# Kernel tuning notes

Measured on AMD Instinct MI355X. Metric: run time of the kernel, lower is better.

Reference implementation:

```python
import jax, jax.numpy as jnp
import numpy as np

EPS = 1e-5
B, C, T = 128, 64, 1000          # batch, EEG channels, time samples
NCLU, HID, NOUT = 8, 512, 4      # clusters, head hidden dim, outputs (=feature_dim)


def _conv1d(x, w):
    # x: (N, Cin, T), w: (Cout, Cin, K), valid conv along time
    return jax.lax.conv_general_dilated(x, w, (1,), 'VALID',
                                        dimension_numbers=('NCH', 'OIH', 'NCH'))


def _bn(x, g, b, m, v):
    # eval-mode BatchNorm over channel dim of (N, C, T)
    return (x - m[None, :, None]) * (g / jnp.sqrt(v + EPS))[None, :, None] + b[None, :, None]


def _pool3(x):
    # maxpool kernel 3 stride 3 along time
    return jax.lax.reduce_window(x, -jnp.inf, jax.lax.max, (1, 1, 3), (1, 1, 3), 'VALID')


def setup_inputs() -> dict:
    key = jax.random.key(0)
    ks = jax.random.split(key, 12)
    def nrm(k, shape, fan):
        return jax.random.normal(k, shape, jnp.float32) / np.float32(np.sqrt(fan))
    inp = {
        'x': jax.random.normal(ks[0], (B, C, T), jnp.float32),
        'cluster_ids': jax.random.randint(ks[1], (B,), 0, NCLU, jnp.int32),
        # Deep4Net-style backbone params
        'w_time': nrm(ks[2], (25, 1, 10), 10),
        'b_time': jnp.zeros((25,), jnp.float32),
        'w_spat': nrm(ks[3], (25, 25, C), 25 * C),
        'w2': nrm(ks[4], (50, 25, 10), 250),
        'w3': nrm(ks[5], (100, 50, 10), 500),
        'w4': nrm(ks[6], (200, 100, 10), 1000),
        'w_cls': nrm(ks[7], (NOUT, 200, 7), 1400),
        'b_cls': jnp.zeros((NOUT,), jnp.float32),
        # per-cluster expert head params
        'hW1': nrm(ks[8], (NCLU, HID, NOUT), NOUT),
        'hb1': jnp.zeros((NCLU, HID), jnp.float32),
        'hW2': nrm(ks[9], (NCLU, NOUT, HID), HID),
        'hb2': jnp.zeros((NCLU, NOUT), jnp.float32),
        'hg': jnp.ones((NCLU, HID), jnp.float32),
        'hbe': jnp.zeros((NCLU, HID), jnp.float32),
        'hm': jnp.zeros((NCLU, HID), jnp.float32),
        'hv': jnp.ones((NCLU, HID), jnp.float32),
    }
    for i, c in zip((1, 2, 3, 4), (25, 50, 100, 200)):
        inp[f'g{i}'] = jnp.ones((c,), jnp.float32)
        inp[f'be{i}'] = jnp.zeros((c,), jnp.float32)
        inp[f'm{i}'] = jnp.zeros((c,), jnp.float32)
        inp[f'v{i}'] = jnp.ones((c,), jnp.float32)
    return inp


def reference(x, cluster_ids, w_time, b_time, w_spat, w2, w3, w4, w_cls, b_cls,
              hW1, hb1, hW2, hb2, hg, hbe, hm, hv,
              g1, be1, m1, v1, g2, be2, m2, v2, g3, be3, m3, v3, g4, be4, m4, v4):
    b_, c_, t_ = x.shape
    # conv_time: same 25 temporal filters applied per EEG channel -> (B, C, 25, T1)
    h = _conv1d(x.reshape(b_ * c_, 1, t_), w_time) + b_time[None, :, None]
    h = h.reshape(b_, c_, 25, -1)
    # conv_spat: collapse EEG channel axis -> (B, 25, T1)
    z = jnp.einsum('bcft,gfc->bgt', h, w_spat)
    z = _pool3(jax.nn.elu(_bn(z, g1, be1, m1, v1)))
    for w, g, be, m, v in ((w2, g2, be2, m2, v2), (w3, g3, be3, m3, v3), (w4, g4, be4, m4, v4)):
        z = _pool3(jax.nn.elu(_bn(_conv1d(z, w), g, be, m, v)))
    # final_conv_length='auto': classifier conv reduces time dim to 1 -> (B, NOUT)
    feats = (_conv1d(z, w_cls) + b_cls[None, :, None])[:, :, 0]
    # per-sample expert head routing (Linear -> BN(eval) -> ReLU -> [Dropout eval] -> Linear)
    h1 = jnp.einsum('bf,bhf->bh', feats, hW1[cluster_ids]) + hb1[cluster_ids]
    h1 = (h1 - hm[cluster_ids]) * (hg[cluster_ids] / jnp.sqrt(hv[cluster_ids] + EPS)) + hbe[cluster_ids]
    h1 = jax.nn.relu(h1)
    return jnp.einsum('bh,boh->bo', h1, hW2[cluster_ids]) + hb2[cluster_ids]
```

## Files before the change

### kernel.cpp

```cpp
#include <hip/hip_runtime.h>
#include <math.h>

#define EPS_BN 1e-5f

typedef __attribute__((ext_vector_type(8))) short short8;
typedef __attribute__((ext_vector_type(4))) float f32x4;
typedef __attribute__((ext_vector_type(4))) unsigned int uint4v;

__device__ __forceinline__ unsigned short f2bf(float f) {
    unsigned int u = __float_as_uint(f);
    u = (u + 0x7fffu + ((u >> 16) & 1u)) >> 16;
    return (unsigned short)u;
}
__device__ __forceinline__ float bf2f(unsigned short s) {
    return __uint_as_float(((unsigned int)s) << 16);
}
__device__ __forceinline__ float elu1(float y) { return y > 0.f ? y : expm1f(y); }
__device__ __forceinline__ float warp_sum(float v) {
    for (int off = 32; off > 0; off >>= 1) v += __shfl_down(v, off);
    return v;
}

#define UW1 0
#define UW2 20480
#define UW3 40960
#define UW4 122880
#define BB1 0
#define BB2 32
#define BB3 96
#define BB4 224
#define Z1G_U 9192320
#define Z2G_U 10544000
#define Z3G_U 11420544

#define RS_ZB 36

__global__ __launch_bounds__(256) void kprep(
    const float* __restrict__ w_time, const float* __restrict__ b_time,
    const float* __restrict__ w_spat,
    const float* __restrict__ w2, const float* __restrict__ w3,
    const float* __restrict__ w4,
    const float* __restrict__ g1, const float* __restrict__ be1,
    const float* __restrict__ m1, const float* __restrict__ v1,
    const float* __restrict__ g2, const float* __restrict__ be2,
    const float* __restrict__ m2, const float* __restrict__ v2,
    const float* __restrict__ g3, const float* __restrict__ be3,
    const float* __restrict__ m3, const float* __restrict__ v3,
    const float* __restrict__ g4, const float* __restrict__ be4,
    const float* __restrict__ m4, const float* __restrict__ v4,
    unsigned short* __restrict__ wsz, float* __restrict__ biasf) {
    int idx = blockIdx.x * 256 + threadIdx.x;
    if (idx < 20480) {
        int k = idx >> 11, g = (idx >> 6) & 31, c = idx & 63;
        float val = 0.f;
        if (g < 25) {
            float s = 0.f;
#pragma unroll
            for (int f = 0; f < 25; ++f)
                s = fmaf(w_spat[g * 1600 + f * 64 + c], w_time[f * 10 + k], s);
            val = s * (g1[g] * rsqrtf(v1[g] + EPS_BN));
        }
        wsz[UW1 + idx] = f2bf(val);
    } else if (idx < 40960) {
        int j = idx - 20480;
        int k = j >> 11, g = (j >> 5) & 63, c = j & 31;
        float val = 0.f;
        if (g < 50 && c < 25)
            val = w2[(g * 25 + c) * 10 + k] * (g2[g] * rsqrtf(v2[g] + EPS_BN));
        wsz[UW2 + j] = f2bf(val);
    } else if (idx < 122880) {
        int j = idx - 40960;
        int k = j >> 13, g = (j >> 6) & 127, c = j & 63;
        float val = 0.f;
        if (g < 100 && c < 50)
            val = w3[(g * 50 + c) * 10 + k] * (g3[g] * rsqrtf(v3[g] + EPS_BN));
        wsz[UW3 + j] = f2bf(val);
    } else if (idx < 409600) {
        int j = idx - 122880;
        int k = j / 28672, r = j % 28672, g = r >> 7, c = r & 127;
        float val = 0.f;
        if (g < 200 && c < 100)
            val = w4[(g * 100 + c) * 10 + k] * (g4[g] * rsqrtf(v4[g] + EPS_BN));
        wsz[UW4 + j] = f2bf(val);
    } else if (idx < 410048) {
        int j = idx - 409600;
        if (j < 32) {
            int g = j; float val = 0.f;
            if (g < 25) {
                float beff = 0.f;
                for (int f = 0; f < 25; ++f) {
                    float a = 0.f;
                    for (int c = 0; c < 64; ++c) a += w_spat[g * 1600 + f * 64 + c];
                    beff = fmaf(a, b_time[f], beff);
                }
                float sc = g1[g] * rsqrtf(v1[g] + EPS_BN);
                val = be1[g] - m1[g] * sc + beff * sc;
            }
            biasf[BB1 + g] = val;
        } else if (j < 96) {
            int g = j - 32; float val = 0.f;
            if (g < 50) { float sc = g2[g] * rsqrtf(v2[g] + EPS_BN); val = be2[g] - m2[g] * sc; }
            biasf[BB2 + g] = val;
        } else if (j < 224) {
            int g = j - 96; float val = 0.f;
            if (g < 100) { float sc = g3[g] * rsqrtf(v3[g] + EPS_BN); val = be3[g] - m3[g] * sc; }
            biasf[BB3 + g] = val;
        } else {
            int g = j - 224; float val = 0.f;
            if (g < 200) { float sc = g4[g] * rsqrtf(v4[g] + EPS_BN); val = be4[g] - m4[g] * sc; }
            biasf[BB4 + g] = val;
        }
    }
}

template<int CPAD, int RS, int SP, int TT, int TPC, int NCHUNK, int JMAX,
         int GPAD, int TPOOL, int GSTORE, int NGV, int OUT_RS, bool OUT_F32,
         int KPRE>
__device__ __forceinline__ void conv_job(
    const unsigned short* xT, const unsigned short* __restrict__ wpk,
    const float* __restrict__ bias,
    unsigned short* zout, float* zoutf, unsigned short* zbw,
    int lane, int gbi, int po0) {
    const int lm = lane & 15, h8 = lane >> 4;
    const int gloc = lane & 31, hh = lane >> 5;

    f32x4 acc[TT][2];
#pragma unroll
    for (int i = 0; i < TT; ++i) {
        acc[i][0] = (f32x4){0.f, 0.f, 0.f, 0.f};
        acc[i][1] = (f32x4){0.f, 0.f, 0.f, 0.f};
    }

    const int abase = lm * RS + h8 * 8;
    const unsigned short* wp = wpk + (gbi * 32 + lm) * CPAD + h8 * 8;
#pragma unroll
    for (int ph = 0; ph < 10 / KPRE; ++ph) {
        short8 w0r[KPRE][SP], w1r[KPRE][SP];
#pragma unroll
        for (int kk = 0; kk < KPRE; ++kk) {
            const int k = ph * KPRE + kk;
#pragma unroll
            for (int s = 0; s < SP; ++s) {
                w0r[kk][s] = *(const short8*)(wp + k * (GPAD * CPAD) + s * 32);
                w1r[kk][s] = *(const short8*)(wp + k * (GPAD * CPAD) + 16 * CPAD + s * 32);
            }
        }
#pragma unroll
        for (int kk = 0; kk < KPRE; ++kk) {
            const int k = ph * KPRE + kk;
#pragma unroll
            for (int s = 0; s < SP; ++s) {
#pragma unroll
                for (int tt = 0; tt < TT; ++tt) {
                    short8 a = *(const short8*)&xT[abase + (tt * 16 + k) * RS + s * 32];
                    acc[tt][0] = __builtin_amdgcn_mfma_f32_16x16x32_bf16(
                        a, w0r[kk][s], acc[tt][0], 0, 0, 0);
                    acc[tt][1] = __builtin_amdgcn_mfma_f32_16x16x32_bf16(
                        a, w1r[kk][s], acc[tt][1], 0, 0, 0);
                }
            }
        }
    }

    const float bv0 = bias[gbi * 32 + lm];
    const float bv1 = bias[gbi * 32 + 16 + lm];
#pragma unroll
    for (int ch = 0; ch < NCHUNK; ++ch) {
#pragma unroll
        for (int ti = 0; ti < TPC; ++ti) {
            int ttg = ch * TPC + ti;
#pragma unroll
            for (int r = 0; r < 4; ++r) {
                float v0 = elu1(acc[ttg][0][r] + bv0);
                float v1 = elu1(acc[ttg][1][r] + bv1);
                int row = ti * 16 + 4 * h8 + r;
                zbw[row * RS_ZB + lm] = f2bf(v0);
                zbw[row * RS_ZB + 16 + lm] = f2bf(v1);
            }
        }
#pragma unroll
        for (int j = 0; j < JMAX; ++j) {
            int po = hh + 2 * j;
            if (3 * po + 2 < TPC * 16) {
                float q0 = bf2f(zbw[(3 * po) * RS_ZB + gloc]);
                float q1 = bf2f(zbw[(3 * po + 1) * RS_ZB + gloc]);
                float q2 = bf2f(zbw[(3 * po + 2) * RS_ZB + gloc]);
                float mx = fmaxf(q0, fmaxf(q1, q2));
                int poa = po0 + ch * 16 + po;
                int ga = gbi * 32 + gloc;
                if (poa < TPOOL && ga < GSTORE) {
                    if constexpr (OUT_F32)
                        zoutf[poa * OUT_RS + ga] = mx;
                    else
                        zout[poa * OUT_RS + ga] =
                            (ga < NGV) ? f2bf(mx) : (unsigned short)0;
                }
            }
        }
    }
}

__global__ __launch_bounds__(64) void ks1(
    const float* __restrict__ x,
    const unsigned short* __restrict__ wsu, const float* __restrict__ biasf,
    unsigned short* __restrict__ wsz) {
    __shared__ __align__(16) unsigned short xT[64 * 72];
    __shared__ __align__(16) unsigned short zb[48 * RS_ZB];
    const int b = blockIdx.x, tci = blockIdx.y, lane = threadIdx.x;
    const int t0 = tci * 48;
    const int cp = lane & 31, hf = lane >> 5;
    const float* xr0 = x + b * 64000 + (2 * cp) * 1000;
    const float* xr1 = xr0 + 1000;
#pragma unroll
    for (int q8 = 0; q8 < 8; ++q8) {
        const int q = hf * 8 + q8;
        const int tg = t0 + 4 * q;
        float4 va = {0.f, 0.f, 0.f, 0.f}, vb = {0.f, 0.f, 0.f, 0.f};
        if (tg + 4 <= 1000) {
            va = *(const float4*)(xr0 + tg);
            vb = *(const float4*)(xr1 + tg);
        } else if (tg < 1000) {
            float* pa = (float*)&va; float* pb = (float*)&vb;
#pragma unroll
            for (int e = 0; e < 4; ++e)
                if (tg + e < 1000) { pa[e] = xr0[tg + e]; pb[e] = xr1[tg + e]; }
        }
        const float* pa = (const float*)&va;
        const float* pb = (const float*)&vb;
#pragma unroll
        for (int e = 0; e < 4; ++e) {
            unsigned int pk = (unsigned int)f2bf(pa[e]) |
                              ((unsigned int)f2bf(pb[e]) << 16);
            *(unsigned int*)&xT[(4 * q + e) * 72 + 2 * cp] = pk;
        }
    }
    __syncthreads();
    conv_job<64, 72, 2, 3, 3, 1, 8, 32, 330, 32, 25, 32, false, 5>(
        xT, wsu + UW1, biasf + BB1,
        wsz + Z1G_U + b * 330 * 32, nullptr, zb, lane, 0, tci * 16);
}

__global__ __launch_bounds__(64) void ks2(
    const unsigned short* __restrict__ wsu, const float* __restrict__ biasf,
    unsigned short* __restrict__ wsz) {
    __shared__ __align__(16) unsigned short xT[64 * 40];
    __shared__ __align__(16) unsigned short zb[48 * RS_ZB];
    const int b = blockIdx.x, y = blockIdx.y, lane = threadIdx.x;
    const int gbi = y / 7, tci = y % 7, t0b = tci * 48;
    const unsigned short* z1g = wsz + Z1G_U + b * 330 * 32;
    for (int idx = lane; idx < 256; idx += 64) {
        int r = idx >> 2, q = idx & 3;
        uint4v v = {0u, 0u, 0u, 0u};
        if (t0b + r < 330) v = *(const uint4v*)&z1g[(t0b + r) * 32 + 8 * q];
        *(uint4v*)&xT[r * 40 + 8 * q] = v;
    }
    __syncthreads();
    conv_job<32, 40, 1, 3, 3, 1, 8, 64, 107, 64, 50, 64, false, 5>(
        xT, wsu + UW2, biasf + BB2,
        wsz + Z2G_U + b * 107 * 64, nullptr, zb, lane, gbi, tci * 16);
}

__global__ __launch_bounds__(64) void ks3(
    const unsigned short* __restrict__ wsu, const float* __restrict__ biasf,
    unsigned short* __restrict__ wsz) {
    __shared__ __align__(16) unsigned short z2t[64 * 72];
    __shared__ __align__(16) unsigned short zb[48 * RS_ZB];
    const int b = blockIdx.x, y = blockIdx.y, lane = threadIdx.x;
    const int gbi = y / 2, tci = y % 2, t0b = tci * 48;
    const unsigned short* z2g = wsz + Z2G_U + b * 107 * 64;
    for (int idx = lane; idx < 512; idx += 64) {
        int r = idx >> 3, q = idx & 7;
        uint4v v = {0u, 0u, 0u, 0u};
        if (t0b + r < 107) v = *(const uint4v*)&z2g[(t0b + r) * 64 + 8 * q];
        *(uint4v*)&z2t[r * 72 + 8 * q] = v;
    }
    __syncthreads();
    conv_job<64, 72, 2, 3, 3, 1, 8, 128, 32, 128, 100, 136, false, 5>(
        z2t, wsu + UW3, biasf + BB3,
        wsz + Z3G_U + b * 44 * 136, nullptr, zb, lane, gbi, tci * 16);
}

__global__ __launch_bounds__(448) void ks4h(
    const unsigned short* __restrict__ wsu, const float* __restrict__ biasf,
    const unsigned short* __restrict__ wsz,
    const float* __restrict__ w_cls, const float* __restrict__ b_cls,
    const int* __restrict__ cid,
    const float* __restrict__ hW1, const float* __restrict__ hb1,
    const float* __restrict__ hW2, const float* __restrict__ hb2,
    const float* __restrict__ hg, const float* __restrict__ hbe,
    const float* __restrict__ hm, const float* __restrict__ hv,
    float* __restrict__ out) {
    __shared__ __align__(16) unsigned short z3t[44 * 136];
    __shared__ __align__(16) unsigned short zb[7 * 32 * RS_ZB];
    __shared__ float z4f[1400];
    __shared__ float feats[4];
    __shared__ float h1s[512];
    const int b = blockIdx.x, t = threadIdx.x;
    const int lane = t & 63, wv = t >> 6;
    const unsigned short* z3g = wsz + Z3G_U + b * 44 * 136;
    for (int idx = t; idx < 748; idx += 448) {
        int r = idx / 17, q = idx % 17;
        uint4v v = {0u, 0u, 0u, 0u};
        if (r < 32) v = *(const uint4v*)&z3g[r * 136 + 8 * q];
        *(uint4v*)&z3t[r * 136 + 8 * q] = v;
    }
    __syncthreads();

    conv_job<128, 136, 4, 2, 2, 1, 4, 224, 7, 200, 200, 200, true, 5>(
        z3t, wsu + UW4, biasf + BB4,
        nullptr, z4f, zb + wv * (32 * RS_ZB), lane, wv, 0);
    __syncthreads();

    if (wv < 4) {
        float p = 0.f;
        for (int i = lane; i < 1400; i += 64) {
            int po = i / 200, g = i - po * 200;
            p = fmaf(z4f[i], w_cls[wv * 1400 + g * 7 + po], p);
        }
        p = warp_sum(p);
        if (lane == 0) feats[wv] = p + b_cls[wv];
    }
    __syncthreads();

    const int c = cid[b];
    const float f0 = feats[0], f1 = feats[1], f2 = feats[2], f3 = feats[3];
    for (int h = t; h < 512; h += 448) {
        const float* w1 = &hW1[(c * 512 + h) * 4];
        float v = f0 * w1[0] + f1 * w1[1] + f2 * w1[2] + f3 * w1[3] + hb1[c * 512 + h];
        float sc = hg[c * 512 + h] * rsqrtf(hv[c * 512 + h] + EPS_BN);
        v = (v - hm[c * 512 + h]) * sc + hbe[c * 512 + h];
        h1s[h] = fmaxf(v, 0.f);
    }
    __syncthreads();
    if (wv < 4) {
        float p = 0.f;
        for (int i = lane; i < 512; i += 64)
            p = fmaf(h1s[i], hW2[(c * 4 + wv) * 512 + i], p);
        p = warp_sum(p);
        if (lane == 0) out[b * 4 + wv] = p + hb2[c * 4 + wv];
    }
}

extern "C" void kernel_launch(void* const* d_in, const int* in_sizes, int n_in,
                              void* d_out, int out_size, void* d_ws, size_t ws_size,
                              hipStream_t stream) {
    const float* x      = (const float*)d_in[0];
    const int*   cid    = (const int*)d_in[1];
    const float* w_time = (const float*)d_in[2];
    const float* b_time = (const float*)d_in[3];
    const float* w_spat = (const float*)d_in[4];
    const float* w2     = (const float*)d_in[5];
    const float* w3     = (const float*)d_in[6];
    const float* w4     = (const float*)d_in[7];
    const float* w_cls  = (const float*)d_in[8];
    const float* b_cls  = (const float*)d_in[9];
    const float* hW1    = (const float*)d_in[10];
    const float* hb1    = (const float*)d_in[11];
    const float* hW2    = (const float*)d_in[12];
    const float* hb2    = (const float*)d_in[13];
    const float* hg     = (const float*)d_in[14];
    const float* hbe    = (const float*)d_in[15];
    const float* hm     = (const float*)d_in[16];
    const float* hv     = (const float*)d_in[17];
    const float* g1  = (const float*)d_in[18];
    const float* be1 = (const float*)d_in[19];
    const float* m1  = (const float*)d_in[20];
    const float* v1  = (const float*)d_in[21];
    const float* g2  = (const float*)d_in[22];
    const float* be2 = (const float*)d_in[23];
    const float* m2  = (const float*)d_in[24];
    const float* v2  = (const float*)d_in[25];
    const float* g3  = (const float*)d_in[26];
    const float* be3 = (const float*)d_in[27];
    const float* m3  = (const float*)d_in[28];
    const float* v3  = (const float*)d_in[29];
    const float* g4  = (const float*)d_in[30];
    const float* be4 = (const float*)d_in[31];
    const float* m4  = (const float*)d_in[32];
    const float* v4  = (const float*)d_in[33];

    unsigned short* wsz = (unsigned short*)d_ws;
    float* biasf = (float*)((char*)d_ws + 819200);
    float* out = (float*)d_out;

    kprep<<<1602, 256, 0, stream>>>(w_time, b_time, w_spat, w2, w3, w4,
                                    g1, be1, m1, v1, g2, be2, m2, v2,
                                    g3, be3, m3, v3, g4, be4, m4, v4,
                                    wsz, biasf);

    ks1<<<dim3(128, 21), 64, 0, stream>>>(x, wsz, biasf, wsz);
    ks2<<<dim3(128, 14), 64, 0, stream>>>(wsz, biasf, wsz);
    ks3<<<dim3(128, 8), 64, 0, stream>>>(wsz, biasf, wsz);
    ks4h<<<128, 448, 0, stream>>>(wsz, biasf, wsz, w_cls, b_cls, cid,
                                  hW1, hb1, hW2, hb2, hg, hbe, hm, hv, out);
}
```

Before: 111.7 us.

## Move input bf16 transpose into prep kernel and have ks1 load pre-transposed tiles

The fp32→bf16 conversion and channel-major to time-major transpose of x moves out of ks1 and into extra blocks of the weight-prep kernel, which transpose through padded shared memory into a global workspace buffer. ks1 then loads its tile with wide 16-byte copies instead of strided float4 reads and per-element packing. This removes redundant overlapping halo reads and the uncoalesced transpose from the conv kernel. In exchange it adds a global round trip of the bf16 input, about 17 MB written and read, and a larger prep launch.

Result: faster. 104.9 us (-6.1%).

```diff
diff --git a/kernel.cpp b/kernel.cpp
--- a/kernel.cpp
+++ b/kernel.cpp
@@ -29,13 +29,16 @@
 #define BB2 32
 #define BB3 96
 #define BB4 224
+#define XTG_U 410496
 #define Z1G_U 9192320
 #define Z2G_U 10544000
 #define Z3G_U 11420544
 
+#define NPREP 1602
 #define RS_ZB 36
 
-__global__ __launch_bounds__(256) void kprep(
+__global__ __launch_bounds__(256) void kprep_tr(
+    const float* __restrict__ x,
     const float* __restrict__ w_time, const float* __restrict__ b_time,
     const float* __restrict__ w_spat,
     const float* __restrict__ w2, const float* __restrict__ w3,
@@ -49,66 +52,103 @@
     const float* __restrict__ g4, const float* __restrict__ be4,
     const float* __restrict__ m4, const float* __restrict__ v4,
     unsigned short* __restrict__ wsz, float* __restrict__ biasf) {
-    int idx = blockIdx.x * 256 + threadIdx.x;
-    if (idx < 20480) {
-        int k = idx >> 11, g = (idx >> 6) & 31, c = idx & 63;
-        float val = 0.f;
-        if (g < 25) {
-            float s = 0.f;
-#pragma unroll
-            for (int f = 0; f < 25; ++f)
-                s = fmaf(w_spat[g * 1600 + f * 64 + c], w_time[f * 10 + k], s);
-            val = s * (g1[g] * rsqrtf(v1[g] + EPS_BN));
-        }
-        wsz[UW1 + idx] = f2bf(val);
-    } else if (idx < 40960) {
-        int j = idx - 20480;
-        int k = j >> 11, g = (j >> 5) & 63, c = j & 31;
-        float val = 0.f;
-        if (g < 50 && c < 25)
-            val = w2[(g * 25 + c) * 10 + k] * (g2[g] * rsqrtf(v2[g] + EPS_BN));
-        wsz[UW2 + j] = f2bf(val);
-    } else if (idx < 122880) {
-        int j = idx - 40960;
-        int k = j >> 13, g = (j >> 6) & 127, c = j & 63;
-        float val = 0.f;
-        if (g < 100 && c < 50)
-            val = w3[(g * 50 + c) * 10 + k] * (g3[g] * rsqrtf(v3[g] + EPS_BN));
-        wsz[UW3 + j] = f2bf(val);
-    } else if (idx < 409600) {
-        int j = idx - 122880;
-        int k = j / 28672, r = j % 28672, g = r >> 7, c = r & 127;
-        float val = 0.f;
-        if (g < 200 && c < 100)
-            val = w4[(g * 100 + c) * 10 + k] * (g4[g] * rsqrtf(v4[g] + EPS_BN));
-        wsz[UW4 + j] = f2bf(val);
-    } else if (idx < 410048) {
-        int j = idx - 409600;
-        if (j < 32) {
-            int g = j; float val = 0.f;
+    __shared__ float tr[64 * 65];
+    if (blockIdx.x < NPREP) {
+        int idx = blockIdx.x * 256 + threadIdx.x;
+        if (idx < 20480) {
+            int k = idx >> 11, g = (idx >> 6) & 31, c = idx & 63;
+            float val = 0.f;
             if (g < 25) {
-                float beff = 0.f;
-                for (int f = 0; f < 25; ++f) {
-                    float a = 0.f;
-                    for (int c = 0; c < 64; ++c) a += w_spat[g * 1600 + f * 64 + c];
-                    beff = fmaf(a, b_time[f], beff);
+                float s = 0.f;
+#pragma unroll
+                for (int f = 0; f < 25; ++f)
+                    s = fmaf(w_spat[g * 1600 + f * 64 + c], w_time[f * 10 + k], s);
+                val = s * (g1[g] * rsqrtf(v1[g] + EPS_BN));
+            }
+            wsz[UW1 + idx] = f2bf(val);
+        } else if (idx < 40960) {
+            int j = idx - 20480;
+            int k = j >> 11, g = (j >> 5) & 63, c = j & 31;
+            float val = 0.f;
+            if (g < 50 && c < 25)
+                val = w2[(g * 25 + c) * 10 + k] * (g2[g] * rsqrtf(v2[g] + EPS_BN));
+            wsz[UW2 + j] = f2bf(val);
+        } else if (idx < 122880) {
+            int j = idx - 40960;
+            int k = j >> 13, g = (j >> 6) & 127, c = j & 63;
+            float val = 0.f;
+            if (g < 100 && c < 50)
+                val = w3[(g * 50 + c) * 10 + k] * (g3[g] * rsqrtf(v3[g] + EPS_BN));
+            wsz[UW3 + j] = f2bf(val);
+        } else if (idx < 409600) {
+            int j = idx - 122880;
+            int k = j / 28672, r = j % 28672, g = r >> 7, c = r & 127;
+            float val = 0.f;
+            if (g < 200 && c < 100)
+                val = w4[(g * 100 + c) * 10 + k] * (g4[g] * rsqrtf(v4[g] + EPS_BN));
+            wsz[UW4 + j] = f2bf(val);
+        } else if (idx < 410048) {
+            int j = idx - 409600;
+            if (j < 32) {
+                int g = j; float val = 0.f;
+                if (g < 25) {
+                    float beff = 0.f;
+                    for (int f = 0; f < 25; ++f) {
+                        float a = 0.f;
+                        for (int c = 0; c < 64; ++c) a += w_spat[g * 1600 + f * 64 + c];
+                        beff = fmaf(a, b_time[f], beff);
+                    }
+                    float sc = g1[g] * rsqrtf(v1[g] + EPS_BN);
+                    val = be1[g] - m1[g] * sc + beff * sc;
                 }
-                float sc = g1[g] * rsqrtf(v1[g] + EPS_BN);
-                val = be1[g] - m1[g] * sc + beff * sc;
-            }
-            biasf[BB1 + g] = val;
-        } else if (j < 96) {
-            int g = j - 32; float val = 0.f;
-            if (g < 50) { float sc = g2[g] * rsqrtf(v2[g] + EPS_BN); val = be2[g] - m2[g] * sc; }
-            biasf[BB2 + g] = val;
-        } else if (j < 224) {
-            int g = j - 96; float val = 0.f;
-            if (g < 100) { float sc = g3[g] * rsqrtf(v3[g] + EPS_BN); val = be3[g] - m3[g] * sc; }
-            biasf[BB3 + g] = val;
-        } else {
-            int g = j - 224; float val = 0.f;
-            if (g < 200) { float sc = g4[g] * rsqrtf(v4[g] + EPS_BN); val = be4[g] - m4[g] * sc; }
-            biasf[BB4 + g] = val;
+                biasf[BB1 + g] = val;
+            } else if (j < 96) {
+                int g = j - 32; float val = 0.f;
+                if (g < 50) { float sc = g2[g] * rsqrtf(v2[g] + EPS_BN); val = be2[g] - m2[g] * sc; }
+                biasf[BB2 + g] = val;
+            } else if (j < 224) {
+                int g = j - 96; float val = 0.f;
+                if (g < 100) { float sc = g3[g] * rsqrtf(v3[g] + EPS_BN); val = be3[g] - m3[g] * sc; }
+                biasf[BB3 + g] = val;
+            } else {
+                int g = j - 224; float val = 0.f;
+                if (g < 200) { float sc = g4[g] * rsqrtf(v4[g] + EPS_BN); val = be4[g] - m4[g] * sc; }
+                biasf[BB4 + g] = val;
+            }
+        }
+    } else {
+        const int bid = blockIdx.x - NPREP;
+        const int b = bid / 17, tile = bid % 17, t = threadIdx.x;
+        const int t0 = tile * 64;
+        const float* xb = x + b * 64000;
+        for (int idx = t; idx < 1024; idx += 256) {
+            int c = idx >> 4, q = idx & 15;
+            int tg = t0 + 4 * q;
+            float4 v = {0.f, 0.f, 0.f, 0.f};
+            if (tg + 4 <= 1000) {
+                v = *(const float4*)(xb + c * 1000 + tg);
+            } else {
+                float* pv = (float*)&v;
+#pragma unroll
+                for (int e = 0; e < 4; ++e)
+                    if (tg + e < 1000) pv[e] = xb[c * 1000 + tg + e];
+            }
+            tr[c * 65 + 4 * q]     = v.x;
+            tr[c * 65 + 4 * q + 1] = v.y;
+            tr[c * 65 + 4 * q + 2] = v.z;
+            tr[c * 65 + 4 * q + 3] = v.w;
+        }
+        __syncthreads();
+        unsigned short* xTg = wsz + XTG_U;
+        for (int idx = t; idx < 2048; idx += 256) {
+            int tl = idx >> 5, cp = idx & 31;
+            int tg = t0 + tl;
+            unsigned int pk = 0u;
+            if (tg < 1000)
+                pk = (unsigned int)f2bf(tr[(2 * cp) * 65 + tl]) |
+                     ((unsigned int)f2bf(tr[(2 * cp + 1) * 65 + tl]) << 16);
+            if (tg < 1072)
+                *(unsigned int*)&xTg[(b * 1072 + tg) * 64 + 2 * cp] = pk;
         }
     }
 }
@@ -201,38 +241,15 @@
 }
 
 __global__ __launch_bounds__(64) void ks1(
-    const float* __restrict__ x,
     const unsigned short* __restrict__ wsu, const float* __restrict__ biasf,
     unsigned short* __restrict__ wsz) {
     __shared__ __align__(16) unsigned short xT[64 * 72];
     __shared__ __align__(16) unsigned short zb[48 * RS_ZB];
     const int b = blockIdx.x, tci = blockIdx.y, lane = threadIdx.x;
-    const int t0 = tci * 48;
-    const int cp = lane & 31, hf = lane >> 5;
-    const float* xr0 = x + b * 64000 + (2 * cp) * 1000;
-    const float* xr1 = xr0 + 1000;
-#pragma unroll
-    for (int q8 = 0; q8 < 8; ++q8) {
-        const int q = hf * 8 + q8;
-        const int tg = t0 + 4 * q;
-        float4 va = {0.f, 0.f, 0.f, 0.f}, vb = {0.f, 0.f, 0.f, 0.f};
-        if (tg + 4 <= 1000) {
-            va = *(const float4*)(xr0 + tg);
-            vb = *(const float4*)(xr1 + tg);
-        } else if (tg < 1000) {
-            float* pa = (float*)&va; float* pb = (float*)&vb;
-#pragma unroll
-            for (int e = 0; e < 4; ++e)
-                if (tg + e < 1000) { pa[e] = xr0[tg + e]; pb[e] = xr1[tg + e]; }
-        }
-        const float* pa = (const float*)&va;
-        const float* pb = (const float*)&vb;
-#pragma unroll
-        for (int e = 0; e < 4; ++e) {
-            unsigned int pk = (unsigned int)f2bf(pa[e]) |
-                              ((unsigned int)f2bf(pb[e]) << 16);
-            *(unsigned int*)&xT[(4 * q + e) * 72 + 2 * cp] = pk;
-        }
+    const unsigned short* xTg = wsz + XTG_U + (b * 1072 + tci * 48) * 64;
+    for (int idx = lane; idx < 512; idx += 64) {
+        int r = idx >> 3, q = idx & 7;
+        *(uint4v*)&xT[r * 72 + 8 * q] = *(const uint4v*)&xTg[r * 64 + 8 * q];
     }
     __syncthreads();
     conv_job<64, 72, 2, 3, 3, 1, 8, 32, 330, 32, 25, 32, false, 5>(
@@ -383,12 +400,12 @@
     float* biasf = (float*)((char*)d_ws + 819200);
     float* out = (float*)d_out;
 
-    kprep<<<1602, 256, 0, stream>>>(w_time, b_time, w_spat, w2, w3, w4,
-                                    g1, be1, m1, v1, g2, be2, m2, v2,
-                                    g3, be3, m3, v3, g4, be4, m4, v4,
-                                    wsz, biasf);
-
-    ks1<<<dim3(128, 21), 64, 0, stream>>>(x, wsz, biasf, wsz);
+    kprep_tr<<<NPREP + 128 * 17, 256, 0, stream>>>(
+        x, w_time, b_time, w_spat, w2, w3, w4,
+        g1, be1, m1, v1, g2, be2, m2, v2, g3, be3, m3, v3, g4, be4, m4, v4,
+        wsz, biasf);
+
+    ks1<<<dim3(128, 21), 64, 0, stream>>>(wsz, biasf, wsz);
     ks2<<<dim3(128, 14), 64, 0, stream>>>(wsz, biasf, wsz);
     ks3<<<dim3(128, 8), 64, 0, stream>>>(wsz, biasf, wsz);
     ks4h<<<128, 448, 0, stream>>>(wsz, biasf, wsz, w_cls, b_cls, cid,
```
